# Kernel tuning notes

Hardware: AMD Instinct MI355X
Metric: run time of the kernel (lower is better)

The kernel has to match this reference:

```python
import jax, jax.numpy as jnp
import numpy as np

FEAT_DIM = 256
DEPTH = 2
N = 8192


def setup_inputs() -> dict:
    key = jax.random.key(0)
    ks = jax.random.split(key, 5)
    bd = 1.0 / FEAT_DIM
    X = jax.random.normal(ks[0], (N, FEAT_DIM), dtype=jnp.float32)
    coefs = jax.random.normal(ks[1], (N,), dtype=jnp.float32)
    linear = jax.random.uniform(ks[2], (DEPTH, FEAT_DIM), minval=-bd, maxval=bd, dtype=jnp.float32)
    dirv = jax.random.uniform(ks[3], (DEPTH, FEAT_DIM), minval=-bd, maxval=bd, dtype=jnp.float32)
    feat = jax.random.uniform(ks[4], (DEPTH, FEAT_DIM), minval=-bd, maxval=bd, dtype=jnp.float32)
    return {"X": X, "coefs": coefs, "linear": linear, "dirv": dirv, "feat": feat}


def reference(X, coefs, linear, dirv, feat):
    # coefs is unused: the torch forward returns before the coef_embed branch.
    emb = X
    n = X.shape[0]
    for i in range(linear.shape[0]):  # depth: small fixed loop
        # torch: emb3[j,a,k] = linear[a]*emb[j,k]; q = sum_a feat[a]*emb3 = (feat.linear)*emb
        a = jnp.dot(feat[i], linear[i])
        b = jnp.dot(dirv[i], linear[i])
        q = a * emb                      # [N, F]
        k = b * emb                      # [N, F]
        k_norm = k / jnp.linalg.norm(k)  # global Frobenius norm, as torch.norm(k)
        inner = jnp.sum(q * k_norm, axis=-1)            # [N]
        scale = jnp.where(inner <= 0, inner, 0.0)       # inner * (inner<=0)
        emb = q - scale[:, None] * k_norm
        # graph_block: X_up[i] = X[i] + (X@X[i]) @ (X - X[i]) / N
        # == X + (S@X - rowsum(S)*X)/N with S = X X^T
        S = emb @ emb.T                                 # [N, N]
        emb = emb + (S @ emb - jnp.sum(S, axis=1, keepdims=True) * emb) / n
    out = jnp.mean(emb @ emb.T, axis=-1)[:-1]           # [N-1]
    return out
```

## Files before the change

kernel.cpp:

```cpp
#include <hip/hip_runtime.h>
#include <math.h>

constexpr int NROW = 8192;
constexpr int FD   = 256;
constexpr int NZ   = 16;

typedef unsigned short u16;
typedef __attribute__((ext_vector_type(8))) short short8;
typedef __attribute__((ext_vector_type(4))) float f32x4;


__device__ __forceinline__ float f_of(float nj, float A, float B, float AB) {
    float inner = AB * nj;
    return A - (inner <= 0.f ? inner : 0.f) * B;
}
__device__ __forceinline__ float wred(float s) {
    #pragma unroll
    for (int off = 32; off; off >>= 1) s += __shfl_xor(s, off);
    return s;
}
__device__ __forceinline__ float dot4(float4 a, float4 b) {
    return a.x*b.x + a.y*b.y + a.z*b.z + a.w*b.w;
}
__device__ __forceinline__ u16 f2bf(float x) {
    unsigned int u = __float_as_uint(x);
    u = (u + 0x7FFFu + ((u >> 16) & 1u)) >> 16;
    return (u16)u;
}

__global__ void k_norm(const float* __restrict__ in, float* __restrict__ nrm,
                       float* __restrict__ fpart) {
    __shared__ float bs[4];
    int wave = threadIdx.x >> 6, lane = threadIdx.x & 63;
    int row = blockIdx.x * 4 + wave;
    const float4 v = *(const float4*)&in[(size_t)row * FD + lane * 4];
    float s = wred(dot4(v, v));
    if (lane == 0) { nrm[row] = s; bs[wave] = s; }
    __syncthreads();
    if (threadIdx.x == 0) fpart[blockIdx.x] = bs[0] + bs[1] + bs[2] + bs[3];
}

__global__ void __launch_bounds__(256, 2)
k_prep(const float* __restrict__ X, const float* __restrict__ nrm0,
       const float* __restrict__ fpart, const float* __restrict__ linear,
       const float* __restrict__ dirv, const float* __restrict__ feat,
       float* __restrict__ scal, float* __restrict__ f0,
       u16* __restrict__ Rbf, u16* __restrict__ Rt, float* __restrict__ cpart) {
    __shared__ u16 T[64][264];
    __shared__ float cred[4][256];
    __shared__ float l[256];
    __shared__ float ff[64];
    __shared__ float sdot[4];
    const int tid = threadIdx.x;
    const int r0 = blockIdx.x * 64;

    if (tid < 64) {
        for (int i = 0; i < 2; ++i) {
            float pa = 0.f, pb = 0.f;
            for (int k = tid; k < FD; k += 64) {
                float ll = linear[i*FD + k];
                pa += feat[i*FD + k] * ll;
                pb += dirv[i*FD + k] * ll;
            }
            pa = wred(pa); pb = wred(pb);
            if (tid == 0) { sdot[i] = pa; sdot[2 + i] = pb; }
        }
    }
    float s = 0.f;
    #pragma unroll
    for (int k = 0; k < 8; ++k) s += fpart[tid + k * 256];
    l[tid] = s;
    __syncthreads();
    for (int off = 128; off; off >>= 1) {
        if (tid < off) l[tid] += l[tid + off];
        __syncthreads();
    }
    const float F2 = l[0];
    const float a = sdot[0], b = sdot[2];
    const float sb = (b > 0.f) ? 1.f : ((b < 0.f) ? -1.f : 0.f);
    const float B = sb / sqrtf(F2);
    const float A = a, AB = a * B;
    if (blockIdx.x == 0 && tid == 0) {
        scal[0] = sdot[0]; scal[1] = sdot[1]; scal[2] = sdot[2]; scal[3] = sdot[3];
        scal[4] = A; scal[5] = B; scal[6] = AB; scal[7] = F2;
    }
    if (tid < 64) {
        float f = f_of(nrm0[r0 + tid], A, B, AB);
        ff[tid] = f;
        f0[r0 + tid] = f;
    }
    __syncthreads();

    const int cg = (tid & 63) * 4;
    const int rg = tid >> 6;
    float4 csum = make_float4(0.f, 0.f, 0.f, 0.f);
    for (int i = 0; i < 16; ++i) {
        int row = rg * 16 + i;
        float4 v = *(const float4*)&X[(size_t)(r0 + row) * FD + cg];
        float f = ff[row];
        v.x *= f; v.y *= f; v.z *= f; v.w *= f;
        csum.x += v.x; csum.y += v.y; csum.z += v.z; csum.w += v.w;
        unsigned lo = (unsigned)f2bf(v.x) | ((unsigned)f2bf(v.y) << 16);
        unsigned hi = (unsigned)f2bf(v.z) | ((unsigned)f2bf(v.w) << 16);
        uint2 pk = make_uint2(lo, hi);
        *(uint2*)&Rbf[(size_t)(r0 + row) * FD + cg] = pk;
        *(uint2*)&T[row][cg] = pk;
    }
    *(float4*)&cred[rg][cg] = csum;
    __syncthreads();
    cpart[(size_t)blockIdx.x * FD + tid] =
        cred[0][tid] + cred[1][tid] + cred[2][tid] + cred[3][tid];

    const int c = tid;
    #pragma unroll
    for (int ch = 0; ch < 8; ++ch) {
        unsigned w0 = (unsigned)T[ch*8+0][c] | ((unsigned)T[ch*8+1][c] << 16);
        unsigned w1 = (unsigned)T[ch*8+2][c] | ((unsigned)T[ch*8+3][c] << 16);
        unsigned w2 = (unsigned)T[ch*8+4][c] | ((unsigned)T[ch*8+5][c] << 16);
        unsigned w3 = (unsigned)T[ch*8+6][c] | ((unsigned)T[ch*8+7][c] << 16);
        uint4 o = make_uint4(w0, w1, w2, w3);
        *(uint4*)&Rt[(size_t)c * NROW + r0 + ch * 8] = o;
    }
}

__global__ void __launch_bounds__(256, 2)
k_gram(const u16* __restrict__ Rt, float* __restrict__ Gp) {
    const int bi = blockIdx.x, bj = blockIdx.y, z = blockIdx.z;
    const int tid = threadIdx.x, w = tid >> 6, lane = tid & 63;
    const int l15 = lane & 15, quad = lane >> 4;
    const int m0 = bi * 64 + (w & 1) * 32;
    const int n0 = bj * 64 + (w >> 1) * 32;
    const size_t kbase = (size_t)z * 512 + quad * 8;
    const u16* am0 = Rt + (size_t)(m0 + l15) * NROW + kbase;
    const u16* am1 = am0 + (size_t)16 * NROW;
    const u16* bn0 = Rt + (size_t)(n0 + l15) * NROW + kbase;
    const u16* bn1 = bn0 + (size_t)16 * NROW;
    f32x4 acc[2][2] = {};
    #pragma unroll
    for (int s = 0; s < 16; ++s) {
        int ko = s * 32;
        short8 a0 = *(const short8*)(am0 + ko);
        short8 a1 = *(const short8*)(am1 + ko);
        short8 b0 = *(const short8*)(bn0 + ko);
        short8 b1 = *(const short8*)(bn1 + ko);
        acc[0][0] = __builtin_amdgcn_mfma_f32_16x16x32_bf16(a0, b0, acc[0][0], 0, 0, 0);
        acc[0][1] = __builtin_amdgcn_mfma_f32_16x16x32_bf16(a0, b1, acc[0][1], 0, 0, 0);
        acc[1][0] = __builtin_amdgcn_mfma_f32_16x16x32_bf16(a1, b0, acc[1][0], 0, 0, 0);
        acc[1][1] = __builtin_amdgcn_mfma_f32_16x16x32_bf16(a1, b1, acc[1][1], 0, 0, 0);
    }
    float* gz = Gp + (size_t)z * (FD * FD);
    #pragma unroll
    for (int mi = 0; mi < 2; ++mi)
        #pragma unroll
        for (int ni = 0; ni < 2; ++ni)
            #pragma unroll
            for (int r = 0; r < 4; ++r)
                gz[(size_t)(m0 + mi*16 + quad*4 + r) * FD + n0 + ni*16 + l15] =
                    acc[mi][ni][r];
}

__global__ void k_gred(const float* __restrict__ Gp, const float* __restrict__ cpart,
                       u16* __restrict__ Gbf, float* __restrict__ c0) {
    int tid = threadIdx.x;
    if (blockIdx.x < 256) {
        size_t e0 = (size_t)blockIdx.x * 256 + tid;
        float s = 0.f;
        #pragma unroll
        for (int z = 0; z < NZ; ++z) s += Gp[(size_t)z * (FD * FD) + e0];
        Gbf[e0] = f2bf(s);
    } else {
        float s = 0.f;
        #pragma unroll 8
        for (int b = 0; b < 128; ++b) s += cpart[(size_t)b * FD + tid];
        c0[tid] = s;
    }
}

__global__ void __launch_bounds__(256, 2)
k_apply(const float* __restrict__ X, const u16* __restrict__ Rbf,
        const u16* __restrict__ Gbf, const float* __restrict__ f0,
        const float* __restrict__ c0, float* __restrict__ emb,
        float* __restrict__ nrm1, float* __restrict__ fpart1,
        float* __restrict__ cpart1, float* __restrict__ wpart1) {
    __shared__ float Sl[32][260];
    __shared__ float u0s[32], ffs[32], nrs[32];
    __shared__ float nw8[32][8];
    const int tid = threadIdx.x, w = tid >> 6, lane = tid & 63;
    const int l15 = lane & 15, quad = lane >> 4;
    const int r0 = blockIdx.x * 32;

    if (tid < 32) ffs[tid] = f0[r0 + tid];
    __syncthreads();
    #pragma unroll
    for (int jj = 0; jj < 8; ++jj) {
        int row = w * 8 + jj;
        float4 xv = *(const float4*)&X[(size_t)(r0 + row) * FD + lane * 4];
        float4 cv = *(const float4*)&c0[lane * 4];
        float t = wred(dot4(xv, cv));
        if (lane == 0) u0s[row] = ffs[row] * t;
    }

    const u16* ap0 = Rbf + (size_t)(r0 + l15) * FD + quad * 8;
    const u16* ap1 = ap0 + (size_t)16 * FD;
    const int n0w = w * 64;
    const u16* bp = Gbf + (size_t)(n0w + l15) * FD + quad * 8;
    f32x4 acc[2][4] = {};
    #pragma unroll
    for (int s = 0; s < 8; ++s) {
        int ko = s * 32;
        short8 a0 = *(const short8*)(ap0 + ko);
        short8 a1 = *(const short8*)(ap1 + ko);
        short8 b0 = *(const short8*)(bp + ko);
        short8 b1 = *(const short8*)(bp + 16 * FD + ko);
        short8 b2 = *(const short8*)(bp + 32 * FD + ko);
        short8 b3 = *(const short8*)(bp + 48 * FD + ko);
        acc[0][0] = __builtin_amdgcn_mfma_f32_16x16x32_bf16(a0, b0, acc[0][0], 0, 0, 0);
        acc[0][1] = __builtin_amdgcn_mfma_f32_16x16x32_bf16(a0, b1, acc[0][1], 0, 0, 0);
        acc[0][2] = __builtin_amdgcn_mfma_f32_16x16x32_bf16(a0, b2, acc[0][2], 0, 0, 0);
        acc[0][3] = __builtin_amdgcn_mfma_f32_16x16x32_bf16(a0, b3, acc[0][3], 0, 0, 0);
        acc[1][0] = __builtin_amdgcn_mfma_f32_16x16x32_bf16(a1, b0, acc[1][0], 0, 0, 0);
        acc[1][1] = __builtin_amdgcn_mfma_f32_16x16x32_bf16(a1, b1, acc[1][1], 0, 0, 0);
        acc[1][2] = __builtin_amdgcn_mfma_f32_16x16x32_bf16(a1, b2, acc[1][2], 0, 0, 0);
        acc[1][3] = __builtin_amdgcn_mfma_f32_16x16x32_bf16(a1, b3, acc[1][3], 0, 0, 0);
    }
    #pragma unroll
    for (int mi = 0; mi < 2; ++mi)
        #pragma unroll
        for (int ni = 0; ni < 4; ++ni)
            #pragma unroll
            for (int r = 0; r < 4; ++r)
                Sl[mi*16 + quad*4 + r][n0w + ni*16 + l15] = acc[mi][ni][r];
    __syncthreads();

    const float invN = 1.0f / NROW;
    float er[32];
    float csum = 0.f;
    #pragma unroll
    for (int j = 0; j < 32; ++j) {
        float x = X[(size_t)(r0 + j) * FD + tid];
        float rv = ffs[j] * x;
        float e = rv + (Sl[j][tid] - u0s[j] * rv) * invN;
        emb[(size_t)(r0 + j) * FD + tid] = e;
        er[j] = e;
        csum += e;
        Sl[j][tid] = e * e;
    }
    __syncthreads();
    {
        int row = tid & 31, q = tid >> 5;
        float pn = 0.f;
        #pragma unroll
        for (int i = 0; i < 32; ++i) pn += Sl[row][q * 32 + i];
        nw8[row][q] = pn;
    }
    __syncthreads();
    if (tid < 32) {
        float nn = 0.f;
        #pragma unroll
        for (int q = 0; q < 8; ++q) nn += nw8[tid][q];
        nrm1[r0 + tid] = nn;
        nrs[tid] = nn;
    }
    __syncthreads();
    float wsum = 0.f;
    #pragma unroll
    for (int j = 0; j < 32; ++j) wsum += nrs[j] * er[j];
    cpart1[(size_t)blockIdx.x * FD + tid] = csum;
    wpart1[(size_t)blockIdx.x * FD + tid] = wsum;
    if (tid == 0) {
        float fp = 0.f;
        #pragma unroll
        for (int j = 0; j < 32; ++j) fp += nrs[j];
        fpart1[blockIdx.x] = fp;
    }
}

__device__ __forceinline__ void red1_scal(const float* fpart1, const float* scal,
                                          float* l, float& A, float& B, float& AB,
                                          float& kap) {
    int tid = threadIdx.x;
    l[tid] = fpart1[tid];
    __syncthreads();
    for (int off = 128; off; off >>= 1) {
        if (tid < off) l[tid] += l[tid + off];
        __syncthreads();
    }
    float F2 = l[0];
    float a = scal[1], b = scal[3];
    float sb = (b > 0.f) ? 1.f : ((b < 0.f) ? -1.f : 0.f);
    B = sb / sqrtf(F2);
    A = a; AB = a * B;
    kap = (AB <= 0.f) ? AB * B : 0.f;
    __syncthreads();
}

__global__ void k_sv(const float* __restrict__ fpart1, const float* __restrict__ scal,
                     const float* __restrict__ cpart1, const float* __restrict__ wpart1,
                     float* __restrict__ svec) {
    __shared__ float l[256];
    float A1, B1, AB1, kap;
    red1_scal(fpart1, scal, l, A1, B1, AB1, kap);
    int tid = threadIdx.x;
    int col = blockIdx.x * 4 + (tid >> 6);
    int lane = tid & 63;
    float cs = 0.f, wsm = 0.f;
    #pragma unroll
    for (int b = lane; b < 256; b += 64) {
        cs  += cpart1[(size_t)b * FD + col];
        wsm += wpart1[(size_t)b * FD + col];
    }
    #pragma unroll
    for (int off = 32; off; off >>= 1) {
        cs  += __shfl_down(cs, off);
        wsm += __shfl_down(wsm, off);
    }
    if (lane == 0) svec[col] = A1 * cs - kap * wsm;
}

__global__ void k_uv(const float* __restrict__ emb, const float* __restrict__ nrm1,
                     const float* __restrict__ scal, const float* __restrict__ fpart1,
                     const float* __restrict__ svec, float* __restrict__ u,
                     float* __restrict__ vpart) {
    __shared__ float l[256];
    __shared__ float ssh[FD];
    __shared__ float uf[16];
    float A, B, AB, kap;
    red1_scal(fpart1, scal, l, A, B, AB, kap);
    int tid = threadIdx.x;
    int r0 = blockIdx.x * 16;
    ssh[tid] = svec[tid];
    __syncthreads();
    const int wave = tid >> 6, lane = tid & 63;
    float4 sv = *(const float4*)&ssh[lane*4];
    #pragma unroll
    for (int jj = 0; jj < 4; ++jj) {
        int row = r0 + wave * 4 + jj;
        float4 ev = *(const float4*)&emb[(size_t)row * FD + lane*4];
        float s = wred(dot4(ev, sv));
        if (lane == 0) {
            float f = A - kap * nrm1[row];
            float uj = f * s;
            u[row] = uj;
            uf[wave*4 + jj] = uj * f;
        }
    }
    __syncthreads();
    float vp = 0.f;
    #pragma unroll
    for (int j = 0; j < 16; ++j)
        vp += uf[j] * emb[(size_t)(r0 + j) * FD + tid];
    vpart[(size_t)blockIdx.x * FD + tid] = vp;
}

__global__ void k_vred(const float* __restrict__ part, float* __restrict__ vec) {
    int tid = threadIdx.x;
    int col = blockIdx.x * 4 + (tid >> 6);
    int lane = tid & 63;
    float s = 0.f;
    #pragma unroll
    for (int b = 0; b < 8; ++b) s += part[(size_t)(b * 64 + lane) * FD + col];
    #pragma unroll
    for (int off = 32; off; off >>= 1) s += __shfl_down(s, off);
    if (lane == 0) vec[col] = s;
}

__global__ void k_out(const float* __restrict__ emb, const float* __restrict__ nrm1,
                      const float* __restrict__ scal, const float* __restrict__ fpart1,
                      const float* __restrict__ vvec, const float* __restrict__ u,
                      float* __restrict__ out) {
    __shared__ float l[256];
    __shared__ float vsh[FD];
    float A, B, AB, kap;
    red1_scal(fpart1, scal, l, A, B, AB, kap);
    int tid = threadIdx.x;
    int r0 = blockIdx.x * 16;
    vsh[tid] = vvec[tid];
    __syncthreads();
    const int wave = tid >> 6, lane = tid & 63;
    const float invN = 1.0f / NROW;
    float4 vv = *(const float4*)&vsh[lane*4];
    #pragma unroll
    for (int jj = 0; jj < 4; ++jj) {
        int row = r0 + wave * 4 + jj;
        float4 ev = *(const float4*)&emb[(size_t)row * FD + lane*4];
        float s = wred(dot4(ev, vv));
        if (lane == 0 && row < NROW - 1) {
            float f = A - kap * nrm1[row];
            float uj = u[row];
            out[row] = (uj + (f * s - uj * uj) * invN) * invN;
        }
    }
}

extern "C" void kernel_launch(void* const* d_in, const int* in_sizes, int n_in,
                              void* d_out, int out_size, void* d_ws, size_t ws_size,
                              hipStream_t stream) {
    const float* X      = (const float*)d_in[0];
    const float* linear = (const float*)d_in[2];
    const float* dirv   = (const float*)d_in[3];
    const float* feat   = (const float*)d_in[4];
    float* out = (float*)d_out;

    char* ws = (char*)d_ws;
    float* scal   = (float*)(ws + 0);
    float* nrm0   = (float*)(ws + 4096);
    float* nrm1   = (float*)(ws + 36864);
    float* fpart  = (float*)(ws + 69632);
    float* fpart1 = (float*)(ws + 77824);
    float* c0     = (float*)(ws + 78848);
    float* svec   = (float*)(ws + 79872);
    float* vvec   = (float*)(ws + 80896);
    float* u      = (float*)(ws + 81920);
    float* f0     = (float*)(ws + 114688);
    float* cpart  = (float*)(ws + 147456);
    u16*   Gbf    = (u16*)  (ws + 278528);
    float* cpart1 = (float*)(ws + 409600);
    float* wpart1 = (float*)(ws + 671744);
    float* vpart  = (float*)(ws + 933888);
    u16*   Rbf    = (u16*)  (ws + 2097152);
    u16*   Rt     = (u16*)  (ws + 6291456);
    float* Gp     = (float*)(ws + 10485760);
    float* emb    = (float*)(ws + 18874368);

    k_norm<<<NROW/4, 256, 0, stream>>>(X, nrm0, fpart);
    k_prep<<<128, 256, 0, stream>>>(X, nrm0, fpart, linear, dirv, feat,
                                    scal, f0, Rbf, Rt, cpart);
    k_gram<<<dim3(4,4,NZ), 256, 0, stream>>>(Rt, Gp);
    k_gred<<<257, 256, 0, stream>>>(Gp, cpart, Gbf, c0);
    k_apply<<<256, 256, 0, stream>>>(X, Rbf, Gbf, f0, c0, emb, nrm1,
                                     fpart1, cpart1, wpart1);
    k_sv<<<64, 256, 0, stream>>>(fpart1, scal, cpart1, wpart1, svec);
    k_uv<<<NROW/16, 256, 0, stream>>>(emb, nrm1, scal, fpart1, svec, u, vpart);
    k_vred<<<64, 256, 0, stream>>>(vpart, vvec);
    k_out<<<NROW/16, 256, 0, stream>>>(emb, nrm1, scal, fpart1, vvec, u, out);
}
```

Before: 127.1 us.

## Fuse all stages into one cooperative persistent kernel with grid syncs

Replaces the nine separate kernel launches with a single cooperative kernel of 256 blocks that runs every stage in sequence, separated by grid-wide barriers. The goal is to remove per-launch overhead and the idle gaps between small kernels. Work is regrouped to 32 rows per block, and the scalar derivation is recomputed redundantly in each block. The multi-kernel path stays as a fallback with shifted workspace offsets. Grid syncs have their own cost, and some phases leave most blocks idle.

```diff
diff --git a/kernel.cpp b/kernel.cpp
--- a/kernel.cpp
+++ b/kernel.cpp
@@ -1,5 +1,8 @@
 #include <hip/hip_runtime.h>
+#include <hip/hip_cooperative_groups.h>
 #include <math.h>
+
+namespace cg = cooperative_groups;
 
 constexpr int NROW = 8192;
 constexpr int FD   = 256;
@@ -9,11 +12,6 @@
 typedef __attribute__((ext_vector_type(8))) short short8;
 typedef __attribute__((ext_vector_type(4))) float f32x4;
 
-
-__device__ __forceinline__ float f_of(float nj, float A, float B, float AB) {
-    float inner = AB * nj;
-    return A - (inner <= 0.f ? inner : 0.f) * B;
-}
 __device__ __forceinline__ float wred(float s) {
     #pragma unroll
     for (int off = 32; off; off >>= 1) s += __shfl_xor(s, off);
@@ -27,6 +25,358 @@
     u = (u + 0x7FFFu + ((u >> 16) & 1u)) >> 16;
     return (u16)u;
 }
+__device__ __forceinline__ float f_of(float nj, float A, float B, float AB) {
+    float inner = AB * nj;
+    return A - (inner <= 0.f ? inner : 0.f) * B;
+}
+
+
+struct P {
+    const float *X, *linear, *dirv, *feat;
+    float* out;
+    float *nrm0, *nrm1, *fpart, *fpart1, *c0, *svec, *vvec, *u;
+    float *cpart, *cpart1, *wpart1, *vpart;
+    u16 *Gbf, *Rbf, *Rt;
+    float *Gp, *emb;
+};
+
+__device__ __forceinline__ void derive(const float* __restrict__ fp, int depth,
+                                       const float* __restrict__ linear,
+                                       const float* __restrict__ dirv,
+                                       const float* __restrict__ feat,
+                                       float* l, float* sdot,
+                                       float& A, float& kap) {
+    int tid = threadIdx.x;
+    if (tid < 64) {
+        for (int i = 0; i < 2; ++i) {
+            float pa = 0.f, pb = 0.f;
+            for (int k = tid; k < FD; k += 64) {
+                float ll = linear[i*FD + k];
+                pa += feat[i*FD + k] * ll;
+                pb += dirv[i*FD + k] * ll;
+            }
+            pa = wred(pa); pb = wred(pb);
+            if (tid == 0) { sdot[i] = pa; sdot[2 + i] = pb; }
+        }
+    }
+    l[tid] = fp[tid];
+    __syncthreads();
+    for (int off = 128; off; off >>= 1) {
+        if (tid < off) l[tid] += l[tid + off];
+        __syncthreads();
+    }
+    float F2 = l[0];
+    float a = sdot[depth], b = sdot[2 + depth];
+    float sb = (b > 0.f) ? 1.f : ((b < 0.f) ? -1.f : 0.f);
+    float B = sb / sqrtf(F2);
+    float AB = a * B;
+    A = a;
+    kap = (AB <= 0.f) ? AB * B : 0.f;
+    __syncthreads();
+}
+
+__global__ void __launch_bounds__(256, 1) mega(P p) {
+    cg::grid_group g = cg::this_grid();
+    extern __shared__ __align__(16) char sh[];
+    const int bid = blockIdx.x, tid = threadIdx.x;
+    const int w = tid >> 6, lane = tid & 63;
+
+    {
+        float* shn = (float*)sh;
+        const int r0 = bid * 32;
+        #pragma unroll
+        for (int jj = 0; jj < 8; ++jj) {
+            int row = r0 + w * 8 + jj;
+            float4 v = *(const float4*)&p.X[(size_t)row * FD + lane * 4];
+            float s = wred(dot4(v, v));
+            if (lane == 0) { p.nrm0[row] = s; shn[w * 8 + jj] = s; }
+        }
+        __syncthreads();
+        if (tid == 0) {
+            float s = 0.f;
+            #pragma unroll
+            for (int j = 0; j < 32; ++j) s += shn[j];
+            p.fpart[bid] = s;
+        }
+    }
+    g.sync();
+
+    {
+        float* l    = (float*)sh;
+        float* sdot = (float*)(sh + 1024);
+        float* ff   = (float*)(sh + 1056);
+        u16 (*T)[264] = (u16(*)[264])(sh + 2048);
+        float (*cred)[256] = (float(*)[256])(sh + 19456);
+        float A, kap;
+        derive(p.fpart, 0, p.linear, p.dirv, p.feat, l, sdot, A, kap);
+        const int r0 = bid * 32;
+        if (tid < 32) ff[tid] = A - kap * p.nrm0[r0 + tid];
+        __syncthreads();
+        const int cg4 = (tid & 63) * 4;
+        const int rg  = tid >> 6;
+        float4 csum = make_float4(0.f, 0.f, 0.f, 0.f);
+        #pragma unroll
+        for (int i = 0; i < 8; ++i) {
+            int row = rg * 8 + i;
+            float4 v = *(const float4*)&p.X[(size_t)(r0 + row) * FD + cg4];
+            float f = ff[row];
+            v.x *= f; v.y *= f; v.z *= f; v.w *= f;
+            csum.x += v.x; csum.y += v.y; csum.z += v.z; csum.w += v.w;
+            unsigned lo = (unsigned)f2bf(v.x) | ((unsigned)f2bf(v.y) << 16);
+            unsigned hi = (unsigned)f2bf(v.z) | ((unsigned)f2bf(v.w) << 16);
+            uint2 pk = make_uint2(lo, hi);
+            *(uint2*)&p.Rbf[(size_t)(r0 + row) * FD + cg4] = pk;
+            *(uint2*)&T[row][cg4] = pk;
+        }
+        *(float4*)&cred[rg][cg4] = csum;
+        __syncthreads();
+        p.cpart[(size_t)bid * FD + tid] =
+            cred[0][tid] + cred[1][tid] + cred[2][tid] + cred[3][tid];
+        const int c = tid;
+        #pragma unroll
+        for (int ch = 0; ch < 4; ++ch) {
+            unsigned w0 = (unsigned)T[ch*8+0][c] | ((unsigned)T[ch*8+1][c] << 16);
+            unsigned w1 = (unsigned)T[ch*8+2][c] | ((unsigned)T[ch*8+3][c] << 16);
+            unsigned w2 = (unsigned)T[ch*8+4][c] | ((unsigned)T[ch*8+5][c] << 16);
+            unsigned w3 = (unsigned)T[ch*8+6][c] | ((unsigned)T[ch*8+7][c] << 16);
+            *(uint4*)&p.Rt[(size_t)c * NROW + r0 + ch * 8] = make_uint4(w0, w1, w2, w3);
+        }
+    }
+    g.sync();
+
+    {
+        const int bi = bid & 3, bj = (bid >> 2) & 3, z = bid >> 4;
+        const int l15 = lane & 15, quad = lane >> 4;
+        const int m0 = bi * 64 + (w & 1) * 32;
+        const int n0 = bj * 64 + (w >> 1) * 32;
+        const size_t kb = (size_t)z * 512 + quad * 8;
+        const u16* am0 = p.Rt + (size_t)(m0 + l15) * NROW + kb;
+        const u16* am1 = am0 + (size_t)16 * NROW;
+        const u16* bn0 = p.Rt + (size_t)(n0 + l15) * NROW + kb;
+        const u16* bn1 = bn0 + (size_t)16 * NROW;
+        f32x4 acc[2][2] = {};
+        #pragma unroll
+        for (int s = 0; s < 16; ++s) {
+            int ko = s * 32;
+            short8 a0 = *(const short8*)(am0 + ko);
+            short8 a1 = *(const short8*)(am1 + ko);
+            short8 b0 = *(const short8*)(bn0 + ko);
+            short8 b1 = *(const short8*)(bn1 + ko);
+            acc[0][0] = __builtin_amdgcn_mfma_f32_16x16x32_bf16(a0, b0, acc[0][0], 0, 0, 0);
+            acc[0][1] = __builtin_amdgcn_mfma_f32_16x16x32_bf16(a0, b1, acc[0][1], 0, 0, 0);
+            acc[1][0] = __builtin_amdgcn_mfma_f32_16x16x32_bf16(a1, b0, acc[1][0], 0, 0, 0);
+            acc[1][1] = __builtin_amdgcn_mfma_f32_16x16x32_bf16(a1, b1, acc[1][1], 0, 0, 0);
+        }
+        float* gz = p.Gp + (size_t)z * FD * FD;
+        #pragma unroll
+        for (int mi = 0; mi < 2; ++mi)
+            #pragma unroll
+            for (int ni = 0; ni < 2; ++ni)
+                #pragma unroll
+                for (int r = 0; r < 4; ++r)
+                    gz[(size_t)(m0 + mi*16 + quad*4 + r) * FD + n0 + ni*16 + l15] =
+                        acc[mi][ni][r];
+    }
+    g.sync();
+
+    {
+        size_t e0 = (size_t)bid * 256 + tid;
+        float s = 0.f;
+        #pragma unroll
+        for (int z = 0; z < NZ; ++z) s += p.Gp[(size_t)z * FD * FD + e0];
+        p.Gbf[e0] = f2bf(s);
+        if (bid < 64) {
+            int col = bid * 4 + (tid >> 6);
+            float cs = 0.f;
+            #pragma unroll
+            for (int b = lane; b < 256; b += 64) cs += p.cpart[(size_t)b * FD + col];
+            cs = wred(cs);
+            if (lane == 0) p.c0[col] = cs;
+        }
+    }
+    g.sync();
+
+    {
+        float (*Sl)[260] = (float(*)[260])sh;
+        float* u0s = (float*)(sh + 33280);
+        float* ffs = (float*)(sh + 33408);
+        float* nrs = (float*)(sh + 33536);
+        float (*nw8)[8] = (float(*)[8])(sh + 33664);
+        float* l    = (float*)(sh + 34688);
+        float* sdot = (float*)(sh + 35712);
+        float A, kap;
+        derive(p.fpart, 0, p.linear, p.dirv, p.feat, l, sdot, A, kap);
+        const int r0 = bid * 32;
+        if (tid < 32) ffs[tid] = A - kap * p.nrm0[r0 + tid];
+        __syncthreads();
+        #pragma unroll
+        for (int jj = 0; jj < 8; ++jj) {
+            int row = w * 8 + jj;
+            float4 xv = *(const float4*)&p.X[(size_t)(r0 + row) * FD + lane * 4];
+            float4 cv = *(const float4*)&p.c0[lane * 4];
+            float t = wred(dot4(xv, cv));
+            if (lane == 0) u0s[row] = ffs[row] * t;
+        }
+        const int l15 = lane & 15, quad = lane >> 4;
+        const u16* ap0 = p.Rbf + (size_t)(r0 + l15) * FD + quad * 8;
+        const u16* ap1 = ap0 + (size_t)16 * FD;
+        const int n0w = w * 64;
+        const u16* bp = p.Gbf + (size_t)(n0w + l15) * FD + quad * 8;
+        f32x4 acc[2][4] = {};
+        #pragma unroll
+        for (int s = 0; s < 8; ++s) {
+            int ko = s * 32;
+            short8 a0 = *(const short8*)(ap0 + ko);
+            short8 a1 = *(const short8*)(ap1 + ko);
+            short8 b0 = *(const short8*)(bp + ko);
+            short8 b1 = *(const short8*)(bp + 16 * FD + ko);
+            short8 b2 = *(const short8*)(bp + 32 * FD + ko);
+            short8 b3 = *(const short8*)(bp + 48 * FD + ko);
+            acc[0][0] = __builtin_amdgcn_mfma_f32_16x16x32_bf16(a0, b0, acc[0][0], 0, 0, 0);
+            acc[0][1] = __builtin_amdgcn_mfma_f32_16x16x32_bf16(a0, b1, acc[0][1], 0, 0, 0);
+            acc[0][2] = __builtin_amdgcn_mfma_f32_16x16x32_bf16(a0, b2, acc[0][2], 0, 0, 0);
+            acc[0][3] = __builtin_amdgcn_mfma_f32_16x16x32_bf16(a0, b3, acc[0][3], 0, 0, 0);
+            acc[1][0] = __builtin_amdgcn_mfma_f32_16x16x32_bf16(a1, b0, acc[1][0], 0, 0, 0);
+            acc[1][1] = __builtin_amdgcn_mfma_f32_16x16x32_bf16(a1, b1, acc[1][1], 0, 0, 0);
+            acc[1][2] = __builtin_amdgcn_mfma_f32_16x16x32_bf16(a1, b2, acc[1][2], 0, 0, 0);
+            acc[1][3] = __builtin_amdgcn_mfma_f32_16x16x32_bf16(a1, b3, acc[1][3], 0, 0, 0);
+        }
+        #pragma unroll
+        for (int mi = 0; mi < 2; ++mi)
+            #pragma unroll
+            for (int ni = 0; ni < 4; ++ni)
+                #pragma unroll
+                for (int r = 0; r < 4; ++r)
+                    Sl[mi*16 + quad*4 + r][n0w + ni*16 + l15] = acc[mi][ni][r];
+        __syncthreads();
+        const float invN = 1.0f / NROW;
+        float er[32];
+        float csum = 0.f;
+        #pragma unroll
+        for (int j = 0; j < 32; ++j) {
+            float x = p.X[(size_t)(r0 + j) * FD + tid];
+            float rv = ffs[j] * x;
+            float e = rv + (Sl[j][tid] - u0s[j] * rv) * invN;
+            p.emb[(size_t)(r0 + j) * FD + tid] = e;
+            er[j] = e;
+            csum += e;
+            Sl[j][tid] = e * e;
+        }
+        __syncthreads();
+        {
+            int row = tid & 31, q = tid >> 5;
+            float pn = 0.f;
+            #pragma unroll
+            for (int i = 0; i < 32; ++i) pn += Sl[row][q * 32 + i];
+            nw8[row][q] = pn;
+        }
+        __syncthreads();
+        if (tid < 32) {
+            float nn = 0.f;
+            #pragma unroll
+            for (int q = 0; q < 8; ++q) nn += nw8[tid][q];
+            p.nrm1[r0 + tid] = nn;
+            nrs[tid] = nn;
+        }
+        __syncthreads();
+        float wsum = 0.f;
+        #pragma unroll
+        for (int j = 0; j < 32; ++j) wsum += nrs[j] * er[j];
+        p.cpart1[(size_t)bid * FD + tid] = csum;
+        p.wpart1[(size_t)bid * FD + tid] = wsum;
+        if (tid == 0) {
+            float fp = 0.f;
+            #pragma unroll
+            for (int j = 0; j < 32; ++j) fp += nrs[j];
+            p.fpart1[bid] = fp;
+        }
+    }
+    g.sync();
+
+    if (bid < 64) {
+        float* l    = (float*)sh;
+        float* sdot = (float*)(sh + 1024);
+        float A1, kap1;
+        derive(p.fpart1, 1, p.linear, p.dirv, p.feat, l, sdot, A1, kap1);
+        int col = bid * 4 + (tid >> 6);
+        float cs = 0.f, wsm = 0.f;
+        #pragma unroll
+        for (int b = lane; b < 256; b += 64) {
+            cs  += p.cpart1[(size_t)b * FD + col];
+            wsm += p.wpart1[(size_t)b * FD + col];
+        }
+        cs = wred(cs); wsm = wred(wsm);
+        if (lane == 0) p.svec[col] = A1 * cs - kap1 * wsm;
+    }
+    g.sync();
+
+    {
+        float* l    = (float*)sh;
+        float* sdot = (float*)(sh + 1024);
+        float* ssh  = (float*)(sh + 2048);
+        float* uf   = (float*)(sh + 3072);
+        float A1, kap1;
+        derive(p.fpart1, 1, p.linear, p.dirv, p.feat, l, sdot, A1, kap1);
+        ssh[tid] = p.svec[tid];
+        __syncthreads();
+        const int r0 = bid * 32;
+        float4 sv4 = *(const float4*)&ssh[lane * 4];
+        #pragma unroll
+        for (int jj = 0; jj < 8; ++jj) {
+            int j = w * 8 + jj, row = r0 + j;
+            float4 ev = *(const float4*)&p.emb[(size_t)row * FD + lane * 4];
+            float s = wred(dot4(ev, sv4));
+            if (lane == 0) {
+                float f = A1 - kap1 * p.nrm1[row];
+                float uj = f * s;
+                p.u[row] = uj;
+                uf[j] = uj * f;
+            }
+        }
+        __syncthreads();
+        float vp = 0.f;
+        #pragma unroll
+        for (int j = 0; j < 32; ++j)
+            vp += uf[j] * p.emb[(size_t)(r0 + j) * FD + tid];
+        p.vpart[(size_t)bid * FD + tid] = vp;
+    }
+    g.sync();
+
+    if (bid < 64) {
+        int col = bid * 4 + (tid >> 6);
+        float s = 0.f;
+        #pragma unroll
+        for (int b = lane; b < 256; b += 64) s += p.vpart[(size_t)b * FD + col];
+        s = wred(s);
+        if (lane == 0) p.vvec[col] = s;
+    }
+    g.sync();
+
+    {
+        float* l    = (float*)sh;
+        float* sdot = (float*)(sh + 1024);
+        float* vsh  = (float*)(sh + 2048);
+        float A1, kap1;
+        derive(p.fpart1, 1, p.linear, p.dirv, p.feat, l, sdot, A1, kap1);
+        vsh[tid] = p.vvec[tid];
+        __syncthreads();
+        const int r0 = bid * 32;
+        const float invN = 1.0f / NROW;
+        float4 vv4 = *(const float4*)&vsh[lane * 4];
+        #pragma unroll
+        for (int jj = 0; jj < 8; ++jj) {
+            int row = r0 + w * 8 + jj;
+            float4 ev = *(const float4*)&p.emb[(size_t)row * FD + lane * 4];
+            float s = wred(dot4(ev, vv4));
+            if (lane == 0 && row < NROW - 1) {
+                float f = A1 - kap1 * p.nrm1[row];
+                float uj = p.u[row];
+                p.out[row] = (uj + (f * s - uj * uj) * invN) * invN;
+            }
+        }
+    }
+}
+
 
 __global__ void k_norm(const float* __restrict__ in, float* __restrict__ nrm,
                        float* __restrict__ fpart) {
@@ -53,7 +403,6 @@
     __shared__ float sdot[4];
     const int tid = threadIdx.x;
     const int r0 = blockIdx.x * 64;
-
     if (tid < 64) {
         for (int i = 0; i < 2; ++i) {
             float pa = 0.f, pb = 0.f;
@@ -90,7 +439,6 @@
         f0[r0 + tid] = f;
     }
     __syncthreads();
-
     const int cg = (tid & 63) * 4;
     const int rg = tid >> 6;
     float4 csum = make_float4(0.f, 0.f, 0.f, 0.f);
@@ -110,7 +458,6 @@
     __syncthreads();
     cpart[(size_t)blockIdx.x * FD + tid] =
         cred[0][tid] + cred[1][tid] + cred[2][tid] + cred[3][tid];
-
     const int c = tid;
     #pragma unroll
     for (int ch = 0; ch < 8; ++ch) {
@@ -188,7 +535,6 @@
     const int tid = threadIdx.x, w = tid >> 6, lane = tid & 63;
     const int l15 = lane & 15, quad = lane >> 4;
     const int r0 = blockIdx.x * 32;
-
     if (tid < 32) ffs[tid] = f0[r0 + tid];
     __syncthreads();
     #pragma unroll
@@ -199,7 +545,6 @@
         float t = wred(dot4(xv, cv));
         if (lane == 0) u0s[row] = ffs[row] * t;
     }
-
     const u16* ap0 = Rbf + (size_t)(r0 + l15) * FD + quad * 8;
     const u16* ap1 = ap0 + (size_t)16 * FD;
     const int n0w = w * 64;
@@ -231,7 +576,6 @@
             for (int r = 0; r < 4; ++r)
                 Sl[mi*16 + quad*4 + r][n0w + ni*16 + l15] = acc[mi][ni][r];
     __syncthreads();
-
     const float invN = 1.0f / NROW;
     float er[32];
     float csum = 0.f;
@@ -400,23 +744,48 @@
     const float* dirv   = (const float*)d_in[3];
     const float* feat   = (const float*)d_in[4];
     float* out = (float*)d_out;
-
     char* ws = (char*)d_ws;
+
+    P p;
+    p.X = X; p.linear = linear; p.dirv = dirv; p.feat = feat; p.out = out;
+    p.nrm0   = (float*)(ws + 4096);
+    p.nrm1   = (float*)(ws + 36864);
+    p.fpart  = (float*)(ws + 69632);
+    p.fpart1 = (float*)(ws + 70656);
+    p.c0     = (float*)(ws + 71680);
+    p.svec   = (float*)(ws + 72704);
+    p.vvec   = (float*)(ws + 73728);
+    p.u      = (float*)(ws + 81920);
+    p.cpart  = (float*)(ws + 131072);
+    p.cpart1 = (float*)(ws + 393216);
+    p.wpart1 = (float*)(ws + 655360);
+    p.vpart  = (float*)(ws + 917504);
+    p.Gbf    = (u16*)  (ws + 1179648);
+    p.Rbf    = (u16*)  (ws + 2097152);
+    p.Rt     = (u16*)  (ws + 6291456);
+    p.Gp     = (float*)(ws + 10485760);
+    p.emb    = (float*)(ws + 18874368);
+
+    void* args[] = { &p };
+    hipError_t err = hipLaunchCooperativeKernel((const void*)mega, dim3(256), dim3(256),
+                                                args, 36864, stream);
+    if (err == hipSuccess) return;
+
     float* scal   = (float*)(ws + 0);
     float* nrm0   = (float*)(ws + 4096);
     float* nrm1   = (float*)(ws + 36864);
-    float* fpart  = (float*)(ws + 69632);
-    float* fpart1 = (float*)(ws + 77824);
-    float* c0     = (float*)(ws + 78848);
-    float* svec   = (float*)(ws + 79872);
-    float* vvec   = (float*)(ws + 80896);
-    float* u      = (float*)(ws + 81920);
-    float* f0     = (float*)(ws + 114688);
-    float* cpart  = (float*)(ws + 147456);
-    u16*   Gbf    = (u16*)  (ws + 278528);
-    float* cpart1 = (float*)(ws + 409600);
-    float* wpart1 = (float*)(ws + 671744);
-    float* vpart  = (float*)(ws + 933888);
+    float* fpart  = (float*)(ws + 69632 + 8192);
+    float* fpart1 = (float*)(ws + 77824 + 8192);
+    float* c0     = (float*)(ws + 78848 + 8192);
+    float* svec   = (float*)(ws + 79872 + 8192);
+    float* vvec   = (float*)(ws + 80896 + 8192);
+    float* u      = (float*)(ws + 90112);
+    float* f0     = (float*)(ws + 122880);
+    float* cpart  = (float*)(ws + 155648);
+    u16*   Gbf    = (u16*)  (ws + 1179648);
+    float* cpart1 = (float*)(ws + 393216);
+    float* wpart1 = (float*)(ws + 655360);
+    float* vpart  = (float*)(ws + 917504);
     u16*   Rbf    = (u16*)  (ws + 2097152);
     u16*   Rt     = (u16*)  (ws + 6291456);
     float* Gp     = (float*)(ws + 10485760);
```

New measurement: 369.3 us. 2.9x slower.

## Fuse Gram split-K reduction into gram kernel and fold c0 sum into apply

Applied to the files above, without the earlier changes.

Rewrites the Gram kernel so each block computes one 16x16 tile with waves splitting K, reducing partials in shared memory and writing bf16 directly, removing the separate reduction kernel and its fp32 partial buffer. The column-sum of cpart is now computed redundantly by every k_apply block instead of in a separate launch. This trades a launch and large partial-buffer traffic for more repeated global loads of Rt panels, a serial single-accumulator MFMA chain, and redundant cpart reads per apply block.

```diff
diff --git a/kernel.cpp b/kernel.cpp
--- a/kernel.cpp
+++ b/kernel.cpp
@@ -3,7 +3,6 @@
 
 constexpr int NROW = 8192;
 constexpr int FD   = 256;
-constexpr int NZ   = 16;
 
 typedef unsigned short u16;
 typedef __attribute__((ext_vector_type(8))) short short8;
@@ -53,7 +52,6 @@
     __shared__ float sdot[4];
     const int tid = threadIdx.x;
     const int r0 = blockIdx.x * 64;
-
     if (tid < 64) {
         for (int i = 0; i < 2; ++i) {
             float pa = 0.f, pb = 0.f;
@@ -90,7 +88,6 @@
         f0[r0 + tid] = f;
     }
     __syncthreads();
-
     const int cg = (tid & 63) * 4;
     const int rg = tid >> 6;
     float4 csum = make_float4(0.f, 0.f, 0.f, 0.f);
@@ -110,7 +107,6 @@
     __syncthreads();
     cpart[(size_t)blockIdx.x * FD + tid] =
         cred[0][tid] + cred[1][tid] + cred[2][tid] + cred[3][tid];
-
     const int c = tid;
     #pragma unroll
     for (int ch = 0; ch < 8; ++ch) {
@@ -124,82 +120,61 @@
 }
 
 __global__ void __launch_bounds__(256, 2)
-k_gram(const u16* __restrict__ Rt, float* __restrict__ Gp) {
-    const int bi = blockIdx.x, bj = blockIdx.y, z = blockIdx.z;
+k_gram(const u16* __restrict__ Rt, u16* __restrict__ Gbf) {
+    __shared__ float part[4][16][17];
+    const int ti = blockIdx.x >> 4, tj = blockIdx.x & 15;
     const int tid = threadIdx.x, w = tid >> 6, lane = tid & 63;
     const int l15 = lane & 15, quad = lane >> 4;
-    const int m0 = bi * 64 + (w & 1) * 32;
-    const int n0 = bj * 64 + (w >> 1) * 32;
-    const size_t kbase = (size_t)z * 512 + quad * 8;
-    const u16* am0 = Rt + (size_t)(m0 + l15) * NROW + kbase;
-    const u16* am1 = am0 + (size_t)16 * NROW;
-    const u16* bn0 = Rt + (size_t)(n0 + l15) * NROW + kbase;
-    const u16* bn1 = bn0 + (size_t)16 * NROW;
-    f32x4 acc[2][2] = {};
-    #pragma unroll
-    for (int s = 0; s < 16; ++s) {
+    const u16* ap = Rt + (size_t)(ti * 16 + l15) * NROW + w * 2048 + quad * 8;
+    const u16* bp = Rt + (size_t)(tj * 16 + l15) * NROW + w * 2048 + quad * 8;
+    f32x4 acc = {};
+    #pragma unroll 8
+    for (int s = 0; s < 64; ++s) {
         int ko = s * 32;
-        short8 a0 = *(const short8*)(am0 + ko);
-        short8 a1 = *(const short8*)(am1 + ko);
-        short8 b0 = *(const short8*)(bn0 + ko);
-        short8 b1 = *(const short8*)(bn1 + ko);
-        acc[0][0] = __builtin_amdgcn_mfma_f32_16x16x32_bf16(a0, b0, acc[0][0], 0, 0, 0);
-        acc[0][1] = __builtin_amdgcn_mfma_f32_16x16x32_bf16(a0, b1, acc[0][1], 0, 0, 0);
-        acc[1][0] = __builtin_amdgcn_mfma_f32_16x16x32_bf16(a1, b0, acc[1][0], 0, 0, 0);
-        acc[1][1] = __builtin_amdgcn_mfma_f32_16x16x32_bf16(a1, b1, acc[1][1], 0, 0, 0);
-    }
-    float* gz = Gp + (size_t)z * (FD * FD);
-    #pragma unroll
-    for (int mi = 0; mi < 2; ++mi)
-        #pragma unroll
-        for (int ni = 0; ni < 2; ++ni)
-            #pragma unroll
-            for (int r = 0; r < 4; ++r)
-                gz[(size_t)(m0 + mi*16 + quad*4 + r) * FD + n0 + ni*16 + l15] =
-                    acc[mi][ni][r];
-}
-
-__global__ void k_gred(const float* __restrict__ Gp, const float* __restrict__ cpart,
-                       u16* __restrict__ Gbf, float* __restrict__ c0) {
-    int tid = threadIdx.x;
-    if (blockIdx.x < 256) {
-        size_t e0 = (size_t)blockIdx.x * 256 + tid;
-        float s = 0.f;
-        #pragma unroll
-        for (int z = 0; z < NZ; ++z) s += Gp[(size_t)z * (FD * FD) + e0];
-        Gbf[e0] = f2bf(s);
-    } else {
-        float s = 0.f;
-        #pragma unroll 8
-        for (int b = 0; b < 128; ++b) s += cpart[(size_t)b * FD + tid];
-        c0[tid] = s;
+        short8 a = *(const short8*)(ap + ko);
+        short8 b = *(const short8*)(bp + ko);
+        acc = __builtin_amdgcn_mfma_f32_16x16x32_bf16(a, b, acc, 0, 0, 0);
+    }
+    #pragma unroll
+    for (int r = 0; r < 4; ++r) part[w][quad * 4 + r][l15] = acc[r];
+    __syncthreads();
+    {
+        int m = tid >> 4, n = tid & 15;
+        float s = part[0][m][n] + part[1][m][n] + part[2][m][n] + part[3][m][n];
+        Gbf[(size_t)(ti * 16 + m) * FD + tj * 16 + n] = f2bf(s);
     }
 }
 
 __global__ void __launch_bounds__(256, 2)
 k_apply(const float* __restrict__ X, const u16* __restrict__ Rbf,
         const u16* __restrict__ Gbf, const float* __restrict__ f0,
-        const float* __restrict__ c0, float* __restrict__ emb,
+        const float* __restrict__ cpart, float* __restrict__ emb,
         float* __restrict__ nrm1, float* __restrict__ fpart1,
         float* __restrict__ cpart1, float* __restrict__ wpart1) {
     __shared__ float Sl[32][260];
+    __shared__ float csh[FD];
     __shared__ float u0s[32], ffs[32], nrs[32];
     __shared__ float nw8[32][8];
     const int tid = threadIdx.x, w = tid >> 6, lane = tid & 63;
     const int l15 = lane & 15, quad = lane >> 4;
     const int r0 = blockIdx.x * 32;
 
+    {
+        float s = 0.f;
+        #pragma unroll 8
+        for (int b = 0; b < 128; ++b) s += cpart[(size_t)b * FD + tid];
+        csh[tid] = s;
+    }
     if (tid < 32) ffs[tid] = f0[r0 + tid];
     __syncthreads();
     #pragma unroll
     for (int jj = 0; jj < 8; ++jj) {
         int row = w * 8 + jj;
         float4 xv = *(const float4*)&X[(size_t)(r0 + row) * FD + lane * 4];
-        float4 cv = *(const float4*)&c0[lane * 4];
+        float4 cv = *(const float4*)&csh[lane * 4];
         float t = wred(dot4(xv, cv));
         if (lane == 0) u0s[row] = ffs[row] * t;
     }
-
     const u16* ap0 = Rbf + (size_t)(r0 + l15) * FD + quad * 8;
     const u16* ap1 = ap0 + (size_t)16 * FD;
     const int n0w = w * 64;
@@ -231,7 +206,6 @@
             for (int r = 0; r < 4; ++r)
                 Sl[mi*16 + quad*4 + r][n0w + ni*16 + l15] = acc[mi][ni][r];
     __syncthreads();
-
     const float invN = 1.0f / NROW;
     float er[32];
     float csum = 0.f;
@@ -407,9 +381,8 @@
     float* nrm1   = (float*)(ws + 36864);
     float* fpart  = (float*)(ws + 69632);
     float* fpart1 = (float*)(ws + 77824);
-    float* c0     = (float*)(ws + 78848);
-    float* svec   = (float*)(ws + 79872);
-    float* vvec   = (float*)(ws + 80896);
+    float* svec   = (float*)(ws + 78848);
+    float* vvec   = (float*)(ws + 79872);
     float* u      = (float*)(ws + 81920);
     float* f0     = (float*)(ws + 114688);
     float* cpart  = (float*)(ws + 147456);
@@ -419,15 +392,13 @@
     float* vpart  = (float*)(ws + 933888);
     u16*   Rbf    = (u16*)  (ws + 2097152);
     u16*   Rt     = (u16*)  (ws + 6291456);
-    float* Gp     = (float*)(ws + 10485760);
     float* emb    = (float*)(ws + 18874368);
 
     k_norm<<<NROW/4, 256, 0, stream>>>(X, nrm0, fpart);
     k_prep<<<128, 256, 0, stream>>>(X, nrm0, fpart, linear, dirv, feat,
                                     scal, f0, Rbf, Rt, cpart);
-    k_gram<<<dim3(4,4,NZ), 256, 0, stream>>>(Rt, Gp);
-    k_gred<<<257, 256, 0, stream>>>(Gp, cpart, Gbf, c0);
-    k_apply<<<256, 256, 0, stream>>>(X, Rbf, Gbf, f0, c0, emb, nrm1,
+    k_gram<<<256, 256, 0, stream>>>(Rt, Gbf);
+    k_apply<<<256, 256, 0, stream>>>(X, Rbf, Gbf, f0, cpart, emb, nrm1,
                                      fpart1, cpart1, wpart1);
     k_sv<<<64, 256, 0, stream>>>(fpart1, scal, cpart1, wpart1, svec);
     k_uv<<<NROW/16, 256, 0, stream>>>(emb, nrm1, scal, fpart1, svec, u, vpart);
```

Measured after the change: 130.7 us. 2.8% more time.
